# Kernel optimization log

Measured on AMD Instinct MI355X. Metric: run time of the kernel, lower is better.

Reference implementation:

```python
import jax, jax.numpy as jnp
import numpy as np

TK, SK = 2, 2
D_MODEL, N_HEADS = 128, 8
NUM_NODES, INPUT_LEN = 207, 12
BATCH = 32
M = TK * SK                 # mask_size
S = 2 ** (M - 1)            # set_size


def _build_masks():
    # masks[i][s] = sorted indices of the other components selected by bitmap s
    masks = []
    for i in range(M):
        row = []
        for s in range(S):
            bits = [int(b) for b in format(s, f'0{M - 1}b')]
            bits.insert(i, 0)
            row.append(np.nonzero(np.array(bits))[0])
        masks.append(row)
    return masks

MASKS = _build_masks()


def setup_inputs() -> dict:
    key = jax.random.key(0)
    k = jax.random.split(key, 8)
    s = 1.0 / np.sqrt(D_MODEL).astype(np.float32)
    return {
        'x': jax.random.normal(k[0], (BATCH, NUM_NODES, INPUT_LEN, TK, SK, D_MODEL), jnp.float32),
        'WQ': jax.random.normal(k[1], (M, D_MODEL, D_MODEL), jnp.float32) * s,
        'bQ': jax.random.normal(k[2], (M, D_MODEL), jnp.float32) * 0.01,
        'WK': jax.random.normal(k[3], (M, D_MODEL, D_MODEL), jnp.float32) * s,
        'bK': jax.random.normal(k[4], (M, D_MODEL), jnp.float32) * 0.01,
        'WV': jax.random.normal(k[5], (M, D_MODEL, D_MODEL), jnp.float32) * s,
        'bV': jax.random.normal(k[6], (M, D_MODEL), jnp.float32) * 0.01,
        'attn_weights': jax.random.normal(k[7], (M, S), jnp.float32),
    }


def _forward(x, WQ, bQ, WK, bK, WV, bV, attn_weights):
    bs = x.shape[0]
    D = x.shape[-1]
    H, dq = N_HEADS, D // N_HEADS
    # (n,v,l,t,s,c) -> (t,s,n,l,v,c) -> (M, bs, L, V, D)
    xr = jnp.transpose(x, (3, 4, 0, 2, 1, 5)).reshape(M, bs, INPUT_LEN, NUM_NODES, D)

    def proj(W, b):
        y = jnp.einsum('ibLVd,ide->ibLVe', xr, W) + b[:, None, None, None, :]
        # -> (M, bs, H, L*V, dq)
        return y.reshape(M, bs, INPUT_LEN * NUM_NODES, H, dq).transpose(0, 1, 3, 2, 4)

    qs, ks, vs = proj(WQ, bQ), proj(WK, bK), proj(WV, bV)
    scale = 1.0 / np.sqrt(dq).astype(np.float32)

    outs = []
    for i in range(M):
        residual = jnp.transpose(xr[i], (0, 2, 1, 3))  # (bs, V, L, D)
        acc = jnp.zeros_like(residual)
        sum_exp = jnp.zeros((), x.dtype)
        for s in range(1, S):
            idx = MASKS[i][s]                 # static subset, size m
            k_sub, v_sub = ks[idx], vs[idx]   # (m, bs, H, n, dq)
            scores = jnp.einsum('bhnd,mbhnd->bhnm', qs[i], k_sub) * scale
            attn = jax.nn.softmax(scores, axis=-1)
            o = jnp.einsum('bhnm,mbhnd->bhnd', attn, v_sub)
            # (bs, n, H, dq) flat -> reshape as in torch: (bs, V, L, D)
            res = o.transpose(0, 2, 1, 3).reshape(bs, NUM_NODES, INPUT_LEN, D)
            w = jnp.exp(attn_weights[i, s])
            acc = acc + res * w
            sum_exp = sum_exp + w
        outs.append(acc / sum_exp + residual)
    out = jnp.stack(outs).transpose(1, 2, 3, 0, 4)  # (bs, V, L, M, D)
    return out.reshape(bs, NUM_NODES, INPUT_LEN, TK, SK, D)


def reference(x, WQ, bQ, WK, bK, WV, bV, attn_weights):
    return _forward(x, WQ, bQ, WK, bK, WV, bV, attn_weights)
```

## Files before the change

### kernel.cpp

```cpp
#include <hip/hip_runtime.h>
#include <hip/hip_bf16.h>

typedef __bf16 bf16_t;
typedef bf16_t bf16x8 __attribute__((ext_vector_type(8)));
typedef float  floatx4 __attribute__((ext_vector_type(4)));

#define NB    32
#define NV    207
#define NL    12
#define NROW  2484
#define TOTROW (NROW * NB)
#define RPB   128
#define NBLK  (TOTROW / RPB)
#define LROWE 136
#define MATE  (16 * LROWE)

__global__ __launch_bounds__(256)
void transpose_w(const float* __restrict__ wq,
                 const float* __restrict__ wk,
                 const float* __restrict__ wv,
                 bf16_t* __restrict__ wt) {
  __shared__ float t[32][33];
  const int mat  = blockIdx.x >> 4;
  const int tile = blockIdx.x & 15;
  const int td = (tile >> 2) << 5;
  const int te = (tile & 3) << 5;
  const float* src = (mat < 4) ? wq : ((mat < 8) ? wk : wv);
  src += ((mat & 3) << 14);
  const int c  = threadIdx.x & 31;
  const int r0 = threadIdx.x >> 5;
#pragma unroll
  for (int rr = 0; rr < 4; ++rr) {
    const int r = r0 + (rr << 3);
    t[r][c] = src[((td + r) << 7) + te + c];
  }
  __syncthreads();
  bf16_t* dst = wt + (mat << 14);
#pragma unroll
  for (int rr = 0; rr < 4; ++rr) {
    const int r = r0 + (rr << 3);
    dst[((te + r) << 7) + td + c] = (bf16_t)t[c][r];
  }
}

__device__ __forceinline__ bf16x8 ldf8(const float* p) {
  floatx4 a = *(const floatx4*)p;
  floatx4 b = *(const floatx4*)(p + 4);
  bf16x8 r;
  r[0] = (bf16_t)a[0]; r[1] = (bf16_t)a[1]; r[2] = (bf16_t)a[2]; r[3] = (bf16_t)a[3];
  r[4] = (bf16_t)b[0]; r[5] = (bf16_t)b[1]; r[6] = (bf16_t)b[2]; r[7] = (bf16_t)b[3];
  return r;
}

__device__ __forceinline__ float bcast(float v) {
  return __uint_as_float(__builtin_amdgcn_readfirstlane(__float_as_uint(v)));
}

__global__ __launch_bounds__(512, 2)
void fused_attn(const float* __restrict__ x,
                const bf16_t* __restrict__ wt,
                const float* __restrict__ bq,
                const float* __restrict__ bk,
                const float* __restrict__ bv,
                const float* __restrict__ aw,
                float* __restrict__ out) {
  __shared__ bf16_t wlds[2][12 * MATE];

  const int tid  = threadIdx.x;
  const int wid  = tid >> 6;
  const int lane = tid & 63;
  const int quad = lane >> 4;
  const int l16  = lane & 15;

  const int g = blockIdx.x * RPB + (wid << 4) + l16;
  const int b = g / NROW;
  const int n = g - b * NROW;
  const int v = n % NV;
  const int l = n / NV;
  const unsigned qkvbase = (((unsigned)b * NROW + (unsigned)(v * NL + l)) << 9);
  const unsigned outbase = ((unsigned)g << 9);

  bf16x8 bx[4][4];
#pragma unroll
  for (int c = 0; c < 4; ++c) {
    const float* xp = x + qkvbase + (c << 7) + (quad << 3);
#pragma unroll
    for (int k = 0; k < 4; ++k) bx[c][k] = ldf8(xp + (k << 5));
  }

  bf16x8 stg[6];
#pragma unroll
  for (int q = 0; q < 6; ++q) {
    const int s = tid + (q << 9);
    stg[q] = *(const bf16x8*)(wt + ((s >> 8) << 14) + (((s >> 4) & 15) << 7) + ((s & 15) << 3));
  }
#pragma unroll
  for (int q = 0; q < 6; ++q) {
    const int s = tid + (q << 9);
    *(bf16x8*)&wlds[0][(s >> 8) * MATE + ((s >> 4) & 15) * LROWE + ((s & 15) << 3)] = stg[q];
  }

  float pw[4][7];
#pragma unroll
  for (int i = 0; i < 4; ++i) {
    float sum = 0.f;
#pragma unroll
    for (int t = 0; t < 7; ++t) { pw[i][t] = __expf(aw[i * 8 + 1 + t]); sum += pw[i][t]; }
    const float inv = __builtin_amdgcn_rcpf(sum);
#pragma unroll
    for (int t = 0; t < 7; ++t) pw[i][t] = bcast(pw[i][t] * inv);
  }

  __syncthreads();

  for (int h = 0; h < 8; ++h) {
    if (h < 7) {
#pragma unroll
      for (int q = 0; q < 6; ++q) {
        const int s = tid + (q << 9);
        stg[q] = *(const bf16x8*)(wt + ((s >> 8) << 14) + ((((h + 1) << 4) + ((s >> 4) & 15)) << 7) + ((s & 15) << 3));
      }
    }

    const int bofs = (h << 4) + (quad << 2);
    const bf16_t* lb = &wlds[h & 1][l16 * LROWE + (quad << 3)];

    floatx4 QQ[4], KK[4], VV[4];
#pragma unroll
    for (int c = 0; c < 4; ++c) {
      {
        const bf16_t* wb = lb + c * MATE;
        const float*  bp = bq + (c << 7) + bofs;
        floatx4 acc; acc[0] = bp[0]; acc[1] = bp[1]; acc[2] = bp[2]; acc[3] = bp[3];
#pragma unroll
        for (int k = 0; k < 4; ++k)
          acc = __builtin_amdgcn_mfma_f32_16x16x32_bf16(*(const bf16x8*)(wb + (k << 5)), bx[c][k], acc, 0, 0, 0);
        QQ[c] = acc;
      }
      {
        const bf16_t* wb = lb + (4 + c) * MATE;
        const float*  bp = bk + (c << 7) + bofs;
        floatx4 acc; acc[0] = bp[0]; acc[1] = bp[1]; acc[2] = bp[2]; acc[3] = bp[3];
#pragma unroll
        for (int k = 0; k < 4; ++k)
          acc = __builtin_amdgcn_mfma_f32_16x16x32_bf16(*(const bf16x8*)(wb + (k << 5)), bx[c][k], acc, 0, 0, 0);
        KK[c] = acc;
      }
      {
        const bf16_t* wb = lb + (8 + c) * MATE;
        const float*  bp = bv + (c << 7) + bofs;
        floatx4 acc; acc[0] = bp[0]; acc[1] = bp[1]; acc[2] = bp[2]; acc[3] = bp[3];
#pragma unroll
        for (int k = 0; k < 4; ++k)
          acc = __builtin_amdgcn_mfma_f32_16x16x32_bf16(*(const bf16x8*)(wb + (k << 5)), bx[c][k], acc, 0, 0, 0);
        VV[c] = acc;
      }
    }

    float ee[4][4];
#pragma unroll
    for (int i = 0; i < 4; ++i) {
#pragma unroll
      for (int j = 0; j < 4; ++j) {
        if (j == i) continue;
        float p = QQ[i][0] * KK[j][0];
        p += QQ[i][1] * KK[j][1];
        p += QQ[i][2] * KK[j][2];
        p += QQ[i][3] * KK[j][3];
        p += __shfl_xor(p, 16);
        p += __shfl_xor(p, 32);
        ee[i][j] = __expf(p * 0.25f);
      }
    }

#pragma unroll
    for (int i = 0; i < 4; ++i) {
      const int ja = (i == 0) ? 1 : 0;
      const int jb = (i < 2) ? 2 : 1;
      const int jc = (i < 3) ? 3 : 2;
      const float* w = pw[i];

      const float ea = ee[i][ja], eb = ee[i][jb], ec = ee[i][jc];
      const float dab = ea + eb, dac = ea + ec, dbc = eb + ec, dabc = dab + ec;
      const float r3 = w[2] * __builtin_amdgcn_rcpf(dbc);
      const float r5 = w[4] * __builtin_amdgcn_rcpf(dac);
      const float r6 = w[5] * __builtin_amdgcn_rcpf(dab);
      const float r7 = w[6] * __builtin_amdgcn_rcpf(dabc);
      const float ca = w[3] + ea * (r5 + r6 + r7);
      const float cb = w[1] + eb * (r3 + r6 + r7);
      const float cc = w[0] + ec * (r3 + r5 + r7);

      const unsigned o = outbase + ((unsigned)i << 7) + (unsigned)bofs;
      const floatx4 res = *(const floatx4*)(x + o);
      floatx4 st;
#pragma unroll
      for (int r = 0; r < 4; ++r)
        st[r] = ca * VV[ja][r] + cb * VV[jb][r] + cc * VV[jc][r] + res[r];
      __builtin_nontemporal_store(st, (floatx4*)(out + o));
    }

    if (h < 7) {
#pragma unroll
      for (int q = 0; q < 6; ++q) {
        const int s = tid + (q << 9);
        *(bf16x8*)&wlds[(h + 1) & 1][(s >> 8) * MATE + ((s >> 4) & 15) * LROWE + ((s & 15) << 3)] = stg[q];
      }
      __syncthreads();
    }
  }
}

extern "C" void kernel_launch(void* const* d_in, const int* in_sizes, int n_in,
                              void* d_out, int out_size, void* d_ws, size_t ws_size,
                              hipStream_t stream) {
  const float* x  = (const float*)d_in[0];
  const float* wq = (const float*)d_in[1];
  const float* bq = (const float*)d_in[2];
  const float* wk = (const float*)d_in[3];
  const float* bk = (const float*)d_in[4];
  const float* wv = (const float*)d_in[5];
  const float* bv = (const float*)d_in[6];
  const float* aw = (const float*)d_in[7];
  float* out = (float*)d_out;
  bf16_t* wt = (bf16_t*)d_ws;

  transpose_w<<<dim3(192), dim3(256), 0, stream>>>(wq, wk, wv, wt);

  fused_attn<<<dim3(NBLK), dim3(512), 0, stream>>>(x, wt, bq, bk, bv, aw, out);
}
```

Before: 374.2 us.

## Single-buffer weight LDS in fragment-major layout and raise occupancy to four blocks

Replaces the double-buffered padded weight tile in shared memory with a single buffer stored in MFMA fragment order, so each lane reads contiguous 16-byte chunks with no bank conflicts and no padding. The LDS footprint drops from about 104 KB to 48 KB per block, and launch bounds ask for four 512-thread blocks per CU instead of two, to hide the latency of the x loads and output stores. Global offsets are precomputed once and reused for every head. The cost is an extra barrier per head before overwriting the shared buffer, plus tighter register limits at the higher occupancy, which could force spills.

After: 494.6 us. 32.2% more time.

```diff
diff --git a/kernel.cpp b/kernel.cpp
--- a/kernel.cpp
+++ b/kernel.cpp
@@ -12,8 +12,6 @@
 #define TOTROW (NROW * NB)
 #define RPB   128
 #define NBLK  (TOTROW / RPB)
-#define LROWE 136
-#define MATE  (16 * LROWE)
 
 __global__ __launch_bounds__(256)
 void transpose_w(const float* __restrict__ wq,
@@ -56,7 +54,7 @@
   return __uint_as_float(__builtin_amdgcn_readfirstlane(__float_as_uint(v)));
 }
 
-__global__ __launch_bounds__(512, 2)
+__global__ __launch_bounds__(512, 4)
 void fused_attn(const float* __restrict__ x,
                 const bf16_t* __restrict__ wt,
                 const float* __restrict__ bq,
@@ -64,7 +62,7 @@
                 const float* __restrict__ bv,
                 const float* __restrict__ aw,
                 float* __restrict__ out) {
-  __shared__ bf16_t wlds[2][12 * MATE];
+  __shared__ bf16_t wlds[12 * 4 * 64 * 8];
 
   const int tid  = threadIdx.x;
   const int wid  = tid >> 6;
@@ -88,17 +86,19 @@
     for (int k = 0; k < 4; ++k) bx[c][k] = ldf8(xp + (k << 5));
   }
 
-  bf16x8 stg[6];
+  unsigned goff[6];
 #pragma unroll
   for (int q = 0; q < 6; ++q) {
     const int s = tid + (q << 9);
-    stg[q] = *(const bf16x8*)(wt + ((s >> 8) << 14) + (((s >> 4) & 15) << 7) + ((s & 15) << 3));
-  }
-#pragma unroll
-  for (int q = 0; q < 6; ++q) {
-    const int s = tid + (q << 9);
-    *(bf16x8*)&wlds[0][(s >> 8) * MATE + ((s >> 4) & 15) * LROWE + ((s & 15) << 3)] = stg[q];
-  }
+    goff[q] = ((unsigned)(s >> 8) << 14) + ((unsigned)(s & 15) << 7)
+            + ((unsigned)((s >> 6) & 3) << 5) + ((unsigned)((s >> 4) & 3) << 3);
+  }
+
+  bf16x8 stg[6];
+#pragma unroll
+  for (int q = 0; q < 6; ++q) stg[q] = *(const bf16x8*)(wt + goff[q]);
+#pragma unroll
+  for (int q = 0; q < 6; ++q) *(bf16x8*)&wlds[(tid << 3) + (q << 12)] = stg[q];
 
   float pw[4][7];
 #pragma unroll
@@ -113,46 +113,45 @@
 
   __syncthreads();
 
+  const bf16_t* lbase = wlds + (lane << 3);
+
   for (int h = 0; h < 8; ++h) {
     if (h < 7) {
 #pragma unroll
-      for (int q = 0; q < 6; ++q) {
-        const int s = tid + (q << 9);
-        stg[q] = *(const bf16x8*)(wt + ((s >> 8) << 14) + ((((h + 1) << 4) + ((s >> 4) & 15)) << 7) + ((s & 15) << 3));
-      }
+      for (int q = 0; q < 6; ++q)
+        stg[q] = *(const bf16x8*)(wt + goff[q] + ((unsigned)(h + 1) << 11));
     }
 
     const int bofs = (h << 4) + (quad << 2);
-    const bf16_t* lb = &wlds[h & 1][l16 * LROWE + (quad << 3)];
 
     floatx4 QQ[4], KK[4], VV[4];
 #pragma unroll
     for (int c = 0; c < 4; ++c) {
       {
-        const bf16_t* wb = lb + c * MATE;
-        const float*  bp = bq + (c << 7) + bofs;
+        const float* bp = bq + (c << 7) + bofs;
         floatx4 acc; acc[0] = bp[0]; acc[1] = bp[1]; acc[2] = bp[2]; acc[3] = bp[3];
 #pragma unroll
         for (int k = 0; k < 4; ++k)
-          acc = __builtin_amdgcn_mfma_f32_16x16x32_bf16(*(const bf16x8*)(wb + (k << 5)), bx[c][k], acc, 0, 0, 0);
+          acc = __builtin_amdgcn_mfma_f32_16x16x32_bf16(
+                  *(const bf16x8*)(lbase + (((c << 2) + k) << 9)), bx[c][k], acc, 0, 0, 0);
         QQ[c] = acc;
       }
       {
-        const bf16_t* wb = lb + (4 + c) * MATE;
-        const float*  bp = bk + (c << 7) + bofs;
+        const float* bp = bk + (c << 7) + bofs;
         floatx4 acc; acc[0] = bp[0]; acc[1] = bp[1]; acc[2] = bp[2]; acc[3] = bp[3];
 #pragma unroll
         for (int k = 0; k < 4; ++k)
-          acc = __builtin_amdgcn_mfma_f32_16x16x32_bf16(*(const bf16x8*)(wb + (k << 5)), bx[c][k], acc, 0, 0, 0);
+          acc = __builtin_amdgcn_mfma_f32_16x16x32_bf16(
+                  *(const bf16x8*)(lbase + ((((4 + c) << 2) + k) << 9)), bx[c][k], acc, 0, 0, 0);
         KK[c] = acc;
       }
       {
-        const bf16_t* wb = lb + (8 + c) * MATE;
-        const float*  bp = bv + (c << 7) + bofs;
+        const float* bp = bv + (c << 7) + bofs;
         floatx4 acc; acc[0] = bp[0]; acc[1] = bp[1]; acc[2] = bp[2]; acc[3] = bp[3];
 #pragma unroll
         for (int k = 0; k < 4; ++k)
-          acc = __builtin_amdgcn_mfma_f32_16x16x32_bf16(*(const bf16x8*)(wb + (k << 5)), bx[c][k], acc, 0, 0, 0);
+          acc = __builtin_amdgcn_mfma_f32_16x16x32_bf16(
+                  *(const bf16x8*)(lbase + ((((8 + c) << 2) + k) << 9)), bx[c][k], acc, 0, 0, 0);
         VV[c] = acc;
       }
     }
@@ -200,11 +199,9 @@
     }
 
     if (h < 7) {
-#pragma unroll
-      for (int q = 0; q < 6; ++q) {
-        const int s = tid + (q << 9);
-        *(bf16x8*)&wlds[(h + 1) & 1][(s >> 8) * MATE + ((s >> 4) & 15) * LROWE + ((s & 15) << 3)] = stg[q];
-      }
+      __syncthreads();
+#pragma unroll
+      for (int q = 0; q < 6; ++q) *(bf16x8*)&wlds[(tid << 3) + (q << 12)] = stg[q];
       __syncthreads();
     }
   }
```
